# Performance work log

Measured on AMD Instinct MI355X. Metric: run time of the kernel, lower is better.

The kernel has to match this reference:

```python
import jax, jax.numpy as jnp
import numpy as np

BALANCE_MOMENTUM = 0.95
BIAS_LR = 0.01
K = 8


def setup_inputs() -> dict:
    key = jax.random.key(0)
    k1, k2 = jax.random.split(key)
    B, S, D, E = 4, 4096, 2048, 64
    return {
        "x": jax.random.normal(k1, (B, S, D), dtype=jnp.float32),
        "gate_w": jax.random.normal(k2, (E, D), dtype=jnp.float32) * (D ** -0.5),
        "expert_bias": jnp.zeros((E,), dtype=jnp.float32),
        "ema_load": jnp.zeros((E,), dtype=jnp.float32),
    }


def reference(x, gate_w, expert_bias, ema_load):
    B, S, D = x.shape
    E = gate_w.shape[0]
    # gate linear (no bias) + learned-free balancing bias
    logits = jnp.einsum("bsd,ed->bse", x, gate_w) + expert_bias  # [B,S,E]
    topk_scores, topk_idx = jax.lax.top_k(logits, K)              # [B,S,K]
    topk_prob = jax.nn.softmax(topk_scores, axis=-1)              # [B,S,K]
    # no-grad load statistics: mean one-hot over (batch, seq)
    counts = jnp.zeros((E,), dtype=x.dtype).at[topk_idx.reshape(-1)].add(1.0)
    load = counts / (B * S)                                       # [E]
    new_ema_load = ema_load * BALANCE_MOMENTUM + load * (1.0 - BALANCE_MOMENTUM)
    target = 1.0 / E
    new_expert_bias = expert_bias + BIAS_LR * (target - new_ema_load)
    return topk_prob, topk_idx, new_expert_bias, new_ema_load
```

## Files before the change

kernel.cpp:

```cpp
#include <hip/hip_runtime.h>
#include <stdint.h>

#define D      2048
#define NE     64
#define TOPK   8
#define BM     64
#define BK     64
#define CHUNKS (D / BK)
#define NTOK   16384
#define PROBS_OFF 0
#define IDX_OFF   131072
#define BIAS_OFF  262144
#define EMA_OFF   262208

__device__ __forceinline__ void gload_lds16(const void* g, void* l) {
  __builtin_amdgcn_global_load_lds(
      (const __attribute__((address_space(1))) void*)g,
      (__attribute__((address_space(3))) void*)l,
      16, 0, 0);
}

__global__ __launch_bounds__(256) void router_main(
    const float* __restrict__ x, const float* __restrict__ gw,
    const float* __restrict__ bias, float* __restrict__ out,
    unsigned* __restrict__ gcnt) {

  __shared__ float xs[2][BM * BK];
  __shared__ float ws[2][NE * BK];
  __shared__ float llds[BM * 65];
  __shared__ unsigned cntL[NE];

  const int tid  = threadIdx.x;
  const int blk  = blockIdx.x;
  const int wave = tid >> 6;
  const int lane = tid & 63;
  const int tx   = tid & 15;
  const int ty   = tid >> 4;

  if (tid < NE) cntL[tid] = 0;

  int aX[4], aW[4];
#pragma unroll
  for (int i = 0; i < 4; ++i) {
    int mm = tx * 4 + i;
    aX[i] = mm * 256 + ((mm >> 2) & 15) * 16;
    int ee = ty * 4 + i;
    aW[i] = ee * 256 + ((ee >> 2) & 15) * 16;
  }

  const float* xsrc = x + (size_t)blk * BM * D;
  const int l16 = lane >> 4;
  const int sct = lane & 15;

  auto stage = [&](int b, int k0) {
#pragma unroll
    for (int ii = 0; ii < 4; ++ii) {
      int q = wave * 4 + ii;
      int row = q * 4 + l16;
      int kk  = k0 + ((sct ^ q) & 15) * 4;
      gload_lds16(xsrc + (size_t)row * D + kk, &xs[b][q * 256]);
      gload_lds16(gw   + (size_t)row * D + kk, &ws[b][q * 256]);
    }
  };

  float acc[4][4];
#pragma unroll
  for (int i = 0; i < 4; ++i)
#pragma unroll
    for (int j = 0; j < 4; ++j) acc[i][j] = 0.0f;

  stage(0, 0);

  for (int c = 0; c < CHUNKS; ++c) {
    __syncthreads();
    if (c + 1 < CHUNKS) stage((c + 1) & 1, (c + 1) * BK);
    const char* xb = (const char*)xs[c & 1];
    const char* wb = (const char*)ws[c & 1];
#pragma unroll
    for (int k4 = 0; k4 < 16; ++k4) {
      float4 xv[4], wv[4];
#pragma unroll
      for (int i = 0; i < 4; ++i)
        xv[i] = *(const float4*)(xb + (aX[i] ^ (k4 << 4)));
#pragma unroll
      for (int j = 0; j < 4; ++j)
        wv[j] = *(const float4*)(wb + (aW[j] ^ (k4 << 4)));
#pragma unroll
      for (int i = 0; i < 4; ++i)
#pragma unroll
        for (int j = 0; j < 4; ++j) {
          acc[i][j] = fmaf(xv[i].x, wv[j].x, acc[i][j]);
          acc[i][j] = fmaf(xv[i].y, wv[j].y, acc[i][j]);
          acc[i][j] = fmaf(xv[i].z, wv[j].z, acc[i][j]);
          acc[i][j] = fmaf(xv[i].w, wv[j].w, acc[i][j]);
        }
    }
  }

  float bj[4];
#pragma unroll
  for (int j = 0; j < 4; ++j) bj[j] = bias[ty * 4 + j];
#pragma unroll
  for (int i = 0; i < 4; ++i)
#pragma unroll
    for (int j = 0; j < 4; ++j)
      llds[(tx * 4 + i) * 65 + (ty * 4 + j)] = acc[i][j] + bj[j];
  __syncthreads();

  if (tid < BM) {
    float v[NE];
#pragma unroll
    for (int e = 0; e < NE; ++e) v[e] = llds[tid * 65 + e];

    unsigned long long used = 0;
    float bv[TOPK];
    int   bi[TOPK];
#pragma unroll
    for (int p = 0; p < TOPK; ++p) {
      float m = -__builtin_inff();
      int mi = 0;
#pragma unroll
      for (int e = 0; e < NE; ++e) {
        bool ok = (((used >> e) & 1ull) == 0ull) && (v[e] > m);
        m  = ok ? v[e] : m;
        mi = ok ? e : mi;
      }
      used |= (1ull << mi);
      bv[p] = m;
      bi[p] = mi;
    }

    float pex[TOPK];
    float s = 0.0f;
#pragma unroll
    for (int p = 0; p < TOPK; ++p) { pex[p] = expf(bv[p] - bv[0]); s += pex[p]; }
    float inv = 1.0f / s;

    int tok = blk * BM + tid;
    float4 o0 = make_float4(pex[0] * inv, pex[1] * inv, pex[2] * inv, pex[3] * inv);
    float4 o1 = make_float4(pex[4] * inv, pex[5] * inv, pex[6] * inv, pex[7] * inv);
    *(float4*)(out + PROBS_OFF + (size_t)tok * 8)     = o0;
    *(float4*)(out + PROBS_OFF + (size_t)tok * 8 + 4) = o1;
    float4 i0 = make_float4((float)bi[0], (float)bi[1], (float)bi[2], (float)bi[3]);
    float4 i1 = make_float4((float)bi[4], (float)bi[5], (float)bi[6], (float)bi[7]);
    *(float4*)(out + IDX_OFF + (size_t)tok * 8)     = i0;
    *(float4*)(out + IDX_OFF + (size_t)tok * 8 + 4) = i1;

#pragma unroll
    for (int p = 0; p < TOPK; ++p) atomicAdd(&cntL[bi[p]], 1u);
  }
  __syncthreads();
  if (tid < NE) atomicAdd(&gcnt[tid], cntL[tid]);
}

__global__ __launch_bounds__(64) void router_finalize(
    const unsigned* __restrict__ gcnt, const float* __restrict__ bias,
    const float* __restrict__ ema, float* __restrict__ out) {
  int e = threadIdx.x;
  float load = (float)gcnt[e] * (1.0f / (float)NTOK);
  float ne = ema[e] * 0.95f + load * 0.05f;
  float nb = bias[e] + 0.01f * (1.0f / 64.0f - ne);
  out[BIAS_OFF + e] = nb;
  out[EMA_OFF + e]  = ne;
}

extern "C" void kernel_launch(void* const* d_in, const int* in_sizes, int n_in,
                              void* d_out, int out_size, void* d_ws, size_t ws_size,
                              hipStream_t stream) {
  const float* x    = (const float*)d_in[0];
  const float* gw   = (const float*)d_in[1];
  const float* bias = (const float*)d_in[2];
  const float* ema  = (const float*)d_in[3];
  float* out = (float*)d_out;
  unsigned* gcnt = (unsigned*)d_ws;

  hipMemsetAsync(d_ws, 0, NE * sizeof(unsigned), stream);
  router_main<<<dim3(NTOK / BM), dim3(256), 0, stream>>>(x, gw, bias, out, gcnt);
  router_finalize<<<dim3(1), dim3(64), 0, stream>>>(gcnt, bias, ema, out);
}
```

Baseline: 273.8 us.

## Split router into weight transpose, split-K register GEMM, and separate top-k kernel

Replaces the single LDS-tiled GEMM+topk kernel with three kernels: a transpose of the gate weights, a split-K GEMM in which each lane owns one token and 16 experts (x read directly from global, wT reads broadcast across lanes), and a separate top-k/softmax kernel that sums the partials. The aim is more blocks in flight (4x grid from split-K) and no LDS staging or block-wide syncs in the GEMM. In exchange it adds partial-sum traffic to global memory (16 MB written and read back), strided per-lane x loads that are poorly coalesced, and two extra launches.

```diff
diff --git a/kernel.cpp b/kernel.cpp
--- a/kernel.cpp
+++ b/kernel.cpp
@@ -4,151 +4,142 @@
 #define D      2048
 #define NE     64
 #define TOPK   8
-#define BM     64
-#define BK     64
-#define CHUNKS (D / BK)
 #define NTOK   16384
+#define KS     4
+#define KCH    (D / KS)
 #define PROBS_OFF 0
 #define IDX_OFF   131072
 #define BIAS_OFF  262144
 #define EMA_OFF   262208
 
-__device__ __forceinline__ void gload_lds16(const void* g, void* l) {
-  __builtin_amdgcn_global_load_lds(
-      (const __attribute__((address_space(1))) void*)g,
-      (__attribute__((address_space(3))) void*)l,
-      16, 0, 0);
+#define WT_OFF   1024
+#define PART_OFF 132096
+
+__global__ __launch_bounds__(256) void wtrans(const float* __restrict__ gw,
+                                              float* __restrict__ wT) {
+  __shared__ float t64[NE][65];
+  const int k0 = blockIdx.x * 64;
+  const int tid = threadIdx.x;
+#pragma unroll
+  for (int r = 0; r < 16; ++r) {
+    int idx = r * 256 + tid;
+    int e = idx >> 6, kk = idx & 63;
+    t64[e][kk] = gw[(size_t)e * D + k0 + kk];
+  }
+  __syncthreads();
+#pragma unroll
+  for (int r = 0; r < 16; ++r) {
+    int idx = r * 256 + tid;
+    int kk = idx >> 6, e = idx & 63;
+    wT[(size_t)(k0 + kk) * NE + e] = t64[e][kk];
+  }
 }
 
-__global__ __launch_bounds__(256) void router_main(
-    const float* __restrict__ x, const float* __restrict__ gw,
-    const float* __restrict__ bias, float* __restrict__ out,
-    unsigned* __restrict__ gcnt) {
-
-  __shared__ float xs[2][BM * BK];
-  __shared__ float ws[2][NE * BK];
-  __shared__ float llds[BM * 65];
-  __shared__ unsigned cntL[NE];
-
+__global__ __launch_bounds__(256) void router_gemm(
+    const float* __restrict__ x, const float* __restrict__ wT,
+    float* __restrict__ partial) {
   const int tid  = threadIdx.x;
-  const int blk  = blockIdx.x;
   const int wave = tid >> 6;
   const int lane = tid & 63;
-  const int tx   = tid & 15;
-  const int ty   = tid >> 4;
+  const int e0   = wave * 16;
+  const int kc   = blockIdx.y;
+  const int tok  = blockIdx.x * 64 + lane;
+  const int kb   = kc * KCH;
 
-  if (tid < NE) cntL[tid] = 0;
+  const float* xp = x + (size_t)tok * D + kb;
 
-  int aX[4], aW[4];
+  float acc[16];
 #pragma unroll
-  for (int i = 0; i < 4; ++i) {
-    int mm = tx * 4 + i;
-    aX[i] = mm * 256 + ((mm >> 2) & 15) * 16;
-    int ee = ty * 4 + i;
-    aW[i] = ee * 256 + ((ee >> 2) & 15) * 16;
-  }
+  for (int j = 0; j < 16; ++j) acc[j] = 0.0f;
 
-  const float* xsrc = x + (size_t)blk * BM * D;
-  const int l16 = lane >> 4;
-  const int sct = lane & 15;
-
-  auto stage = [&](int b, int k0) {
+#pragma unroll 2
+  for (int k4 = 0; k4 < KCH / 4; ++k4) {
+    float4 xv = *(const float4*)(xp + k4 * 4);
 #pragma unroll
-    for (int ii = 0; ii < 4; ++ii) {
-      int q = wave * 4 + ii;
-      int row = q * 4 + l16;
-      int kk  = k0 + ((sct ^ q) & 15) * 4;
-      gload_lds16(xsrc + (size_t)row * D + kk, &xs[b][q * 256]);
-      gload_lds16(gw   + (size_t)row * D + kk, &ws[b][q * 256]);
-    }
-  };
-
-  float acc[4][4];
-#pragma unroll
-  for (int i = 0; i < 4; ++i)
-#pragma unroll
-    for (int j = 0; j < 4; ++j) acc[i][j] = 0.0f;
-
-  stage(0, 0);
-
-  for (int c = 0; c < CHUNKS; ++c) {
-    __syncthreads();
-    if (c + 1 < CHUNKS) stage((c + 1) & 1, (c + 1) * BK);
-    const char* xb = (const char*)xs[c & 1];
-    const char* wb = (const char*)ws[c & 1];
-#pragma unroll
-    for (int k4 = 0; k4 < 16; ++k4) {
-      float4 xv[4], wv[4];
-#pragma unroll
-      for (int i = 0; i < 4; ++i)
-        xv[i] = *(const float4*)(xb + (aX[i] ^ (k4 << 4)));
-#pragma unroll
-      for (int j = 0; j < 4; ++j)
-        wv[j] = *(const float4*)(wb + (aW[j] ^ (k4 << 4)));
-#pragma unroll
-      for (int i = 0; i < 4; ++i)
-#pragma unroll
-        for (int j = 0; j < 4; ++j) {
-          acc[i][j] = fmaf(xv[i].x, wv[j].x, acc[i][j]);
-          acc[i][j] = fmaf(xv[i].y, wv[j].y, acc[i][j]);
-          acc[i][j] = fmaf(xv[i].z, wv[j].z, acc[i][j]);
-          acc[i][j] = fmaf(xv[i].w, wv[j].w, acc[i][j]);
-        }
+    for (int i = 0; i < 4; ++i) {
+      const float* wr = wT + (size_t)(kb + k4 * 4 + i) * NE + e0;
+      float4 wa = *(const float4*)(wr);
+      float4 wb = *(const float4*)(wr + 4);
+      float4 wc = *(const float4*)(wr + 8);
+      float4 wd = *(const float4*)(wr + 12);
+      float xk = (i == 0) ? xv.x : (i == 1) ? xv.y : (i == 2) ? xv.z : xv.w;
+      acc[0]  = fmaf(xk, wa.x, acc[0]);
+      acc[1]  = fmaf(xk, wa.y, acc[1]);
+      acc[2]  = fmaf(xk, wa.z, acc[2]);
+      acc[3]  = fmaf(xk, wa.w, acc[3]);
+      acc[4]  = fmaf(xk, wb.x, acc[4]);
+      acc[5]  = fmaf(xk, wb.y, acc[5]);
+      acc[6]  = fmaf(xk, wb.z, acc[6]);
+      acc[7]  = fmaf(xk, wb.w, acc[7]);
+      acc[8]  = fmaf(xk, wc.x, acc[8]);
+      acc[9]  = fmaf(xk, wc.y, acc[9]);
+      acc[10] = fmaf(xk, wc.z, acc[10]);
+      acc[11] = fmaf(xk, wc.w, acc[11]);
+      acc[12] = fmaf(xk, wd.x, acc[12]);
+      acc[13] = fmaf(xk, wd.y, acc[13]);
+      acc[14] = fmaf(xk, wd.z, acc[14]);
+      acc[15] = fmaf(xk, wd.w, acc[15]);
     }
   }
 
-  float bj[4];
 #pragma unroll
-  for (int j = 0; j < 4; ++j) bj[j] = bias[ty * 4 + j];
-#pragma unroll
-  for (int i = 0; i < 4; ++i)
-#pragma unroll
-    for (int j = 0; j < 4; ++j)
-      llds[(tx * 4 + i) * 65 + (ty * 4 + j)] = acc[i][j] + bj[j];
+  for (int j = 0; j < 16; ++j)
+    partial[(size_t)(kc * NE + e0 + j) * NTOK + tok] = acc[j];
+}
+
+__global__ __launch_bounds__(128) void router_topk(
+    const float* __restrict__ partial, const float* __restrict__ bias,
+    float* __restrict__ out, unsigned* __restrict__ gcnt) {
+  __shared__ unsigned cntL[NE];
+  const int tid = threadIdx.x;
+  const int t   = blockIdx.x * 128 + tid;
+  if (tid < NE) cntL[tid] = 0;
   __syncthreads();
 
-  if (tid < BM) {
-    float v[NE];
+  float v[NE];
 #pragma unroll
-    for (int e = 0; e < NE; ++e) v[e] = llds[tid * 65 + e];
+  for (int e = 0; e < NE; ++e) v[e] = bias[e];
+#pragma unroll
+  for (int p = 0; p < KS; ++p)
+#pragma unroll
+    for (int e = 0; e < NE; ++e)
+      v[e] += partial[(size_t)(p * NE + e) * NTOK + t];
 
-    unsigned long long used = 0;
-    float bv[TOPK];
-    int   bi[TOPK];
+  unsigned long long used = 0;
+  float bv[TOPK];
+  int   bi[TOPK];
 #pragma unroll
-    for (int p = 0; p < TOPK; ++p) {
-      float m = -__builtin_inff();
-      int mi = 0;
+  for (int p = 0; p < TOPK; ++p) {
+    float m = -__builtin_inff();
+    int mi = 0;
 #pragma unroll
-      for (int e = 0; e < NE; ++e) {
-        bool ok = (((used >> e) & 1ull) == 0ull) && (v[e] > m);
-        m  = ok ? v[e] : m;
-        mi = ok ? e : mi;
-      }
-      used |= (1ull << mi);
-      bv[p] = m;
-      bi[p] = mi;
+    for (int e = 0; e < NE; ++e) {
+      bool ok = (((used >> e) & 1ull) == 0ull) && (v[e] > m);
+      m  = ok ? v[e] : m;
+      mi = ok ? e : mi;
     }
+    used |= (1ull << mi);
+    bv[p] = m;
+    bi[p] = mi;
+  }
 
-    float pex[TOPK];
-    float s = 0.0f;
+  float pex[TOPK];
+  float s = 0.0f;
 #pragma unroll
-    for (int p = 0; p < TOPK; ++p) { pex[p] = expf(bv[p] - bv[0]); s += pex[p]; }
-    float inv = 1.0f / s;
+  for (int p = 0; p < TOPK; ++p) { pex[p] = expf(bv[p] - bv[0]); s += pex[p]; }
+  float inv = 1.0f / s;
 
-    int tok = blk * BM + tid;
-    float4 o0 = make_float4(pex[0] * inv, pex[1] * inv, pex[2] * inv, pex[3] * inv);
-    float4 o1 = make_float4(pex[4] * inv, pex[5] * inv, pex[6] * inv, pex[7] * inv);
-    *(float4*)(out + PROBS_OFF + (size_t)tok * 8)     = o0;
-    *(float4*)(out + PROBS_OFF + (size_t)tok * 8 + 4) = o1;
-    float4 i0 = make_float4((float)bi[0], (float)bi[1], (float)bi[2], (float)bi[3]);
-    float4 i1 = make_float4((float)bi[4], (float)bi[5], (float)bi[6], (float)bi[7]);
-    *(float4*)(out + IDX_OFF + (size_t)tok * 8)     = i0;
-    *(float4*)(out + IDX_OFF + (size_t)tok * 8 + 4) = i1;
+  float4 o0 = make_float4(pex[0] * inv, pex[1] * inv, pex[2] * inv, pex[3] * inv);
+  float4 o1 = make_float4(pex[4] * inv, pex[5] * inv, pex[6] * inv, pex[7] * inv);
+  *(float4*)(out + PROBS_OFF + (size_t)t * 8)     = o0;
+  *(float4*)(out + PROBS_OFF + (size_t)t * 8 + 4) = o1;
+  float4 i0 = make_float4((float)bi[0], (float)bi[1], (float)bi[2], (float)bi[3]);
+  float4 i1 = make_float4((float)bi[4], (float)bi[5], (float)bi[6], (float)bi[7]);
+  *(float4*)(out + IDX_OFF + (size_t)t * 8)     = i0;
+  *(float4*)(out + IDX_OFF + (size_t)t * 8 + 4) = i1;
 
 #pragma unroll
-    for (int p = 0; p < TOPK; ++p) atomicAdd(&cntL[bi[p]], 1u);
-  }
+  for (int p = 0; p < TOPK; ++p) atomicAdd(&cntL[bi[p]], 1u);
   __syncthreads();
   if (tid < NE) atomicAdd(&gcnt[tid], cntL[tid]);
 }
@@ -172,9 +163,14 @@
   const float* bias = (const float*)d_in[2];
   const float* ema  = (const float*)d_in[3];
   float* out = (float*)d_out;
+  float* wsf = (float*)d_ws;
   unsigned* gcnt = (unsigned*)d_ws;
+  float* wT      = wsf + WT_OFF;
+  float* partial = wsf + PART_OFF;
 
   hipMemsetAsync(d_ws, 0, NE * sizeof(unsigned), stream);
-  router_main<<<dim3(NTOK / BM), dim3(256), 0, stream>>>(x, gw, bias, out, gcnt);
+  wtrans<<<dim3(D / 64), dim3(256), 0, stream>>>(gw, wT);
+  router_gemm<<<dim3(NTOK / 64, KS), dim3(256), 0, stream>>>(x, wT, partial);
+  router_topk<<<dim3(NTOK / 128), dim3(128), 0, stream>>>(partial, bias, out, gcnt);
   router_finalize<<<dim3(1), dim3(64), 0, stream>>>(gcnt, bias, ema, out);
 }
```

Result: slower. 512.4 us (+87.1%).
